# Kernel tuning notes

Measured on AMD Instinct MI355X. Metric: run time of the kernel, lower is better.

The kernel has to match this reference:

```python
import jax, jax.numpy as jnp
import numpy as np

EPS = 1e-7
MAX_TANH = 1.0 - 1e-6  # clamp for arctanh stability


def _norm(v):
    # last-axis L2 norm, clamped away from zero
    return jnp.maximum(jnp.linalg.norm(v, axis=-1, keepdims=True), EPS)


def log_map_zero(y):
    # Poincare ball (c=1) log map at the origin
    n = _norm(y)
    return jnp.arctanh(jnp.clip(n, 0.0, MAX_TANH)) * y / n


def exp_map_zero(v):
    # Poincare ball (c=1) exp map at the origin
    n = _norm(v)
    return jnp.tanh(n) * v / n


def h_add(x, y):
    # Mobius addition x (+) y on the Poincare ball (c=1)
    xy = jnp.sum(x * y, axis=-1, keepdims=True)
    x2 = jnp.sum(x * x, axis=-1, keepdims=True)
    y2 = jnp.sum(y * y, axis=-1, keepdims=True)
    num = (1.0 + 2.0 * xy + y2) * x + (1.0 - x2) * y
    den = 1.0 + 2.0 * xy + x2 * y2
    return num / jnp.maximum(den, EPS)


def h_mul(x, W):
    # Mobius matrix-vector multiply: exp0( log0(x) @ W )
    return exp_map_zero(log_map_zero(x) @ W)


def setup_inputs() -> dict:
    key = jax.random.key(0)
    k1, k2, k3, k4 = jax.random.split(key, 4)
    N, F_IN, F_OUT = 8192, 128, 128
    # node features inside the unit ball: ||x|| ~ 0.05*sqrt(128) ~ 0.57
    x = 0.05 * jax.random.normal(k1, (N, F_IN), dtype=jnp.float32)
    # sparse-ish row-normalized dense adjacency
    a = (jax.random.uniform(k2, (N, N)) < 0.01).astype(jnp.float32)
    adj = a / jnp.maximum(a.sum(axis=1, keepdims=True), 1.0)
    # xavier-uniform-ish weights
    lim_e = np.sqrt(6.0 / (F_IN + F_IN)) * np.sqrt(2.0)
    lim_l = np.sqrt(6.0 / (2 * F_IN + F_OUT)) * np.sqrt(2.0)
    embed = jax.random.uniform(k3, (F_IN, F_IN), minval=-lim_e, maxval=lim_e, dtype=jnp.float32)
    layer = jax.random.uniform(k4, (2 * F_IN, F_OUT), minval=-lim_l, maxval=lim_l, dtype=jnp.float32)
    embed_bias = jnp.zeros((F_IN,), dtype=jnp.float32)
    layer_bias = jnp.zeros((F_OUT,), dtype=jnp.float32)
    return {"x": x, "adj": adj, "embed": embed, "layer": layer,
            "embed_bias": embed_bias, "layer_bias": layer_bias}


def reference(x, adj, embed, layer, embed_bias, layer_bias):
    # h = (embed (x)mobius x) (+) embed_bias
    h = h_mul(x, embed)                      # [N, F_IN]
    h = h_add(h, embed_bias[None, :])
    # neighbor aggregation in tangent space at origin
    neigh = exp_map_zero(adj @ log_map_zero(h))   # [N, F_IN]
    # out = (layer (x)mobius [x ; neigh]) (+) layer_bias
    out = h_mul(jnp.concatenate((x, neigh), axis=1), layer)  # [N, F_OUT]
    out = h_add(out, layer_bias[None, :])
    return out
```

## Files before the change

### kernel.cpp

```cpp
#include <hip/hip_runtime.h>
#include <math.h>

#define EPS  1e-7f
#define MAXT 0.999999f

typedef short  s16x8  __attribute__((ext_vector_type(8)));
typedef float  f32x16 __attribute__((ext_vector_type(16)));

__device__ __forceinline__ float waveRedSum(float v) {
    #pragma unroll
    for (int off = 32; off > 0; off >>= 1)
        v += __shfl_xor(v, off, 64);
    return v;
}

__device__ __forceinline__ unsigned short f2bf(float f) {
    unsigned u = __float_as_uint(f);
    u += 0x7fff + ((u >> 16) & 1);
    return (unsigned short)(u >> 16);
}

__global__ __launch_bounds__(256) void kA(const float* __restrict__ x,
                                          const float* __restrict__ embed,
                                          const float* __restrict__ ebias,
                                          unsigned short* __restrict__ vpack) {
    __shared__ float u[4][128];
    const int wave = threadIdx.x >> 6;
    const int lane = threadIdx.x & 63;
    const int row  = blockIdx.x * 4 + wave;
    const int c0   = lane * 2;

    const float2 xr = *(const float2*)(x + (size_t)row * 128 + c0);

    float n2 = waveRedSum(xr.x * xr.x + xr.y * xr.y);
    float n  = fmaxf(sqrtf(n2), EPS);
    float sc = atanhf(fminf(n, MAXT)) / n;
    u[wave][c0]     = xr.x * sc;
    u[wave][c0 + 1] = xr.y * sc;
    __syncthreads();

    float a0 = 0.f, a1 = 0.f;
    #pragma unroll 8
    for (int k = 0; k < 128; k++) {
        float  uk = u[wave][k];
        float2 e  = *(const float2*)(embed + (size_t)k * 128 + c0);
        a0 = fmaf(uk, e.x, a0);
        a1 = fmaf(uk, e.y, a1);
    }

    float np2 = waveRedSum(a0 * a0 + a1 * a1);
    float np  = fmaxf(sqrtf(np2), EPS);
    float se  = tanhf(np) / np;
    float h0 = a0 * se, h1 = a1 * se;
    float x2 = np2 * se * se;

    float bx = ebias[c0], by = ebias[c0 + 1];
    float xy = waveRedSum(h0 * bx + h1 * by);
    float y2 = waveRedSum(bx * bx + by * by);
    float den = fmaxf(1.f + 2.f * xy + x2 * y2, EPS);
    float cx = 1.f + 2.f * xy + y2;
    float cy = 1.f - x2;
    float hb0 = (cx * h0 + cy * bx) / den;
    float hb1 = (cx * h1 + cy * by) / den;

    float m2 = waveRedSum(hb0 * hb0 + hb1 * hb1);
    float m  = fmaxf(sqrtf(m2), EPS);
    float sl = atanhf(fminf(m, MAXT)) / m;
    float v0 = hb0 * sl, v1 = hb1 * sl;

    const int tbase = (row >> 4) * 2048 + (row & 15);
    vpack[tbase + c0 * 16]       = f2bf(v0);
    vpack[tbase + (c0 + 1) * 16] = f2bf(v1);
}

__device__ __forceinline__ void kb_chunk(const float4& ca0, const float4& ca1,
                                         const unsigned short* bp,
                                         f32x16& acc0, f32x16& acc1,
                                         f32x16& acc2, f32x16& acc3) {
    s16x8 b0 = *(const s16x8*)(bp);
    s16x8 b1 = *(const s16x8*)(bp + 32 * 16);
    s16x8 b2 = *(const s16x8*)(bp + 64 * 16);
    s16x8 b3 = *(const s16x8*)(bp + 96 * 16);
    union { unsigned short u[8]; s16x8 v; } af;
    af.u[0] = f2bf(ca0.x); af.u[1] = f2bf(ca0.y);
    af.u[2] = f2bf(ca0.z); af.u[3] = f2bf(ca0.w);
    af.u[4] = f2bf(ca1.x); af.u[5] = f2bf(ca1.y);
    af.u[6] = f2bf(ca1.z); af.u[7] = f2bf(ca1.w);
    acc0 = __builtin_amdgcn_mfma_f32_32x32x16_bf16(af.v, b0, acc0, 0, 0, 0);
    acc1 = __builtin_amdgcn_mfma_f32_32x32x16_bf16(af.v, b1, acc1, 0, 0, 0);
    acc2 = __builtin_amdgcn_mfma_f32_32x32x16_bf16(af.v, b2, acc2, 0, 0, 0);
    acc3 = __builtin_amdgcn_mfma_f32_32x32x16_bf16(af.v, b3, acc3, 0, 0, 0);
}

__global__ __launch_bounds__(256) void kB(const float* __restrict__ adj,
                                          const unsigned short* __restrict__ vpack,
                                          float* __restrict__ tpart,
                                          int klen) {
    const int wave = threadIdx.x >> 6;
    const int lane = threadIdx.x & 63;
    const int rt   = blockIdx.x * 4 + wave;
    const int r0   = rt * 32;
    const int k0   = blockIdx.y * klen;
    float* tout    = tpart + (size_t)blockIdx.y * (8192 * 128);

    const int m  = lane & 31;
    const int kh = lane >> 5;

    const float* aptr = adj + (size_t)(r0 + m) * 8192 + k0 + kh * 8;
    const unsigned short* bbase = vpack + (size_t)(k0 >> 4) * 2048 + m * 16 + kh * 8;

    f32x16 acc0 = {0.f}, acc1 = {0.f}, acc2 = {0.f}, acc3 = {0.f};

    const int kiters = klen >> 4;

    float4 a0 = *(const float4*)(aptr);
    float4 a1 = *(const float4*)(aptr + 4);

    for (int kt = 0; kt < kiters - 1; ++kt) {
        float4 ca0 = a0, ca1 = a1;
        aptr += 16;
        a0 = *(const float4*)(aptr);
        a1 = *(const float4*)(aptr + 4);
        kb_chunk(ca0, ca1, bbase + (size_t)kt * 2048, acc0, acc1, acc2, acc3);
    }
    kb_chunk(a0, a1, bbase + (size_t)(kiters - 1) * 2048, acc0, acc1, acc2, acc3);

    #pragma unroll
    for (int r = 0; r < 16; ++r) {
        int row  = r0 + (r & 3) + 8 * (r >> 2) + 4 * kh;
        float* o = tout + (size_t)row * 128 + m;
        o[0]  = acc0[r];
        o[32] = acc1[r];
        o[64] = acc2[r];
        o[96] = acc3[r];
    }
}

__global__ __launch_bounds__(256) void kC(const float* __restrict__ x,
                                          const float* __restrict__ tpart,
                                          const float* __restrict__ layer,
                                          const float* __restrict__ lbias,
                                          float* __restrict__ out,
                                          int S) {
    __shared__ float w[4][256];
    const int wave = threadIdx.x >> 6;
    const int lane = threadIdx.x & 63;
    const int row  = blockIdx.x * 4 + wave;
    const int c0   = lane * 2;

    float2 tr = *(const float2*)(tpart + (size_t)row * 128 + c0);
    for (int s = 1; s < S; s++) {
        float2 p = *(const float2*)(tpart + (size_t)s * 8192 * 128 + (size_t)row * 128 + c0);
        tr.x += p.x; tr.y += p.y;
    }
    const float2 xr = *(const float2*)(x + (size_t)row * 128 + c0);

    float st = waveRedSum(tr.x * tr.x + tr.y * tr.y);
    float sx = waveRedSum(xr.x * xr.x + xr.y * xr.y);

    float nt = fmaxf(sqrtf(st), EPS);
    float se = tanhf(nt) / nt;

    float ncat2 = sx + st * se * se;
    float ncat  = fmaxf(sqrtf(ncat2), EPS);
    float sw    = atanhf(fminf(ncat, MAXT)) / ncat;
    w[wave][c0]           = xr.x * sw;
    w[wave][c0 + 1]       = xr.y * sw;
    w[wave][128 + c0]     = tr.x * se * sw;
    w[wave][128 + c0 + 1] = tr.y * se * sw;
    __syncthreads();

    float a0 = 0.f, a1 = 0.f;
    #pragma unroll 8
    for (int k = 0; k < 256; k++) {
        float  wk = w[wave][k];
        float2 e  = *(const float2*)(layer + (size_t)k * 128 + c0);
        a0 = fmaf(wk, e.x, a0);
        a1 = fmaf(wk, e.y, a1);
    }

    float np2 = waveRedSum(a0 * a0 + a1 * a1);
    float np  = fmaxf(sqrtf(np2), EPS);
    float so  = tanhf(np) / np;
    float o0 = a0 * so, o1 = a1 * so;
    float x2 = np2 * so * so;

    float bx = lbias[c0], by = lbias[c0 + 1];
    float xy = waveRedSum(o0 * bx + o1 * by);
    float y2 = waveRedSum(bx * bx + by * by);
    float den = fmaxf(1.f + 2.f * xy + x2 * y2, EPS);
    float cx = 1.f + 2.f * xy + y2;
    float cy = 1.f - x2;

    float2 res;
    res.x = (cx * o0 + cy * bx) / den;
    res.y = (cx * o1 + cy * by) / den;
    *(float2*)(out + (size_t)row * 128 + c0) = res;
}

extern "C" void kernel_launch(void* const* d_in, const int* in_sizes, int n_in,
                              void* d_out, int out_size, void* d_ws, size_t ws_size,
                              hipStream_t stream) {
    const float* x     = (const float*)d_in[0];
    const float* adj   = (const float*)d_in[1];
    const float* embed = (const float*)d_in[2];
    const float* layer = (const float*)d_in[3];
    const float* eb    = (const float*)d_in[4];
    const float* lb    = (const float*)d_in[5];
    float* out = (float*)d_out;

    const size_t vbytes = (size_t)8192 * 128 * 2;
    const size_t slice  = (size_t)8192 * 128 * 4;

    int S = 1;
    if      (ws_size >= vbytes + 16 * slice) S = 16;
    else if (ws_size >= vbytes +  8 * slice) S = 8;
    else if (ws_size >= vbytes +  4 * slice) S = 4;
    else if (ws_size >= vbytes +  2 * slice) S = 2;

    unsigned short* vpack = (unsigned short*)d_ws;
    float* tpart = (float*)((char*)d_ws + vbytes);

    kA<<<2048, 256, 0, stream>>>(x, embed, eb, vpack);
    kB<<<dim3(64, S), 256, 0, stream>>>(adj, vpack, tpart, 8192 / S);
    kC<<<2048, 256, 0, stream>>>(x, tpart, layer, lb, out, S);
}
```

Before: 519.5 us.

## Deepen kB software pipeline with multi-stage A/B prefetch and cap split-K at 8

Rewrites the kB inner loop to keep four adjacency chunks and two B chunks in flight in registers, unrolled by four, so global-load latency is hidden behind the MFMAs. The fp32-to-bf16 conversion now uses the packed __float22bfloat162_rn intrinsic in place of manual per-element rounding. The split-K factor is capped at 8, which halves the partial-sum traffic in kC but gives kB fewer blocks. The change raises register pressure, and at the tail it issues redundant clamped loads.

New measurement: 530.3 us. 1.02x slower.

```diff
diff --git a/kernel.cpp b/kernel.cpp
--- a/kernel.cpp
+++ b/kernel.cpp
@@ -1,4 +1,5 @@
 #include <hip/hip_runtime.h>
+#include <hip/hip_bf16.h>
 #include <math.h>
 
 #define EPS  1e-7f
@@ -6,6 +7,7 @@
 
 typedef short  s16x8  __attribute__((ext_vector_type(8)));
 typedef float  f32x16 __attribute__((ext_vector_type(16)));
+typedef float  f32x4  __attribute__((ext_vector_type(4)));
 
 __device__ __forceinline__ float waveRedSum(float v) {
     #pragma unroll
@@ -73,23 +75,13 @@
     vpack[tbase + (c0 + 1) * 16] = f2bf(v1);
 }
 
-__device__ __forceinline__ void kb_chunk(const float4& ca0, const float4& ca1,
-                                         const unsigned short* bp,
-                                         f32x16& acc0, f32x16& acc1,
-                                         f32x16& acc2, f32x16& acc3) {
-    s16x8 b0 = *(const s16x8*)(bp);
-    s16x8 b1 = *(const s16x8*)(bp + 32 * 16);
-    s16x8 b2 = *(const s16x8*)(bp + 64 * 16);
-    s16x8 b3 = *(const s16x8*)(bp + 96 * 16);
-    union { unsigned short u[8]; s16x8 v; } af;
-    af.u[0] = f2bf(ca0.x); af.u[1] = f2bf(ca0.y);
-    af.u[2] = f2bf(ca0.z); af.u[3] = f2bf(ca0.w);
-    af.u[4] = f2bf(ca1.x); af.u[5] = f2bf(ca1.y);
-    af.u[6] = f2bf(ca1.z); af.u[7] = f2bf(ca1.w);
-    acc0 = __builtin_amdgcn_mfma_f32_32x32x16_bf16(af.v, b0, acc0, 0, 0, 0);
-    acc1 = __builtin_amdgcn_mfma_f32_32x32x16_bf16(af.v, b1, acc1, 0, 0, 0);
-    acc2 = __builtin_amdgcn_mfma_f32_32x32x16_bf16(af.v, b2, acc2, 0, 0, 0);
-    acc3 = __builtin_amdgcn_mfma_f32_32x32x16_bf16(af.v, b3, acc3, 0, 0, 0);
+__device__ __forceinline__ s16x8 pack_bf16x8(const f32x4 a, const f32x4 b) {
+    union { __hip_bfloat162 h[4]; s16x8 v; } r;
+    r.h[0] = __float22bfloat162_rn({a.x, a.y});
+    r.h[1] = __float22bfloat162_rn({a.z, a.w});
+    r.h[2] = __float22bfloat162_rn({b.x, b.y});
+    r.h[3] = __float22bfloat162_rn({b.z, b.w});
+    return r.v;
 }
 
 __global__ __launch_bounds__(256) void kB(const float* __restrict__ adj,
@@ -106,24 +98,55 @@
     const int m  = lane & 31;
     const int kh = lane >> 5;
 
-    const float* aptr = adj + (size_t)(r0 + m) * 8192 + k0 + kh * 8;
+    const float* abase = adj + (size_t)(r0 + m) * 8192 + k0 + kh * 8;
     const unsigned short* bbase = vpack + (size_t)(k0 >> 4) * 2048 + m * 16 + kh * 8;
 
+    const int kiters = klen >> 4;
+
     f32x16 acc0 = {0.f}, acc1 = {0.f}, acc2 = {0.f}, acc3 = {0.f};
 
-    const int kiters = klen >> 4;
-
-    float4 a0 = *(const float4*)(aptr);
-    float4 a1 = *(const float4*)(aptr + 4);
-
-    for (int kt = 0; kt < kiters - 1; ++kt) {
-        float4 ca0 = a0, ca1 = a1;
-        aptr += 16;
-        a0 = *(const float4*)(aptr);
-        a1 = *(const float4*)(aptr + 4);
-        kb_chunk(ca0, ca1, bbase + (size_t)kt * 2048, acc0, acc1, acc2, acc3);
-    }
-    kb_chunk(a0, a1, bbase + (size_t)(kiters - 1) * 2048, acc0, acc1, acc2, acc3);
+    f32x4 aq[4][2];
+    s16x8 bq[2][4];
+
+    #pragma unroll
+    for (int c = 0; c < 4; ++c) {
+        aq[c][0] = *(const f32x4*)(abase + c * 16);
+        aq[c][1] = *(const f32x4*)(abase + c * 16 + 4);
+    }
+    #pragma unroll
+    for (int c = 0; c < 2; ++c) {
+        const unsigned short* bp = bbase + (size_t)c * 2048;
+        bq[c][0] = *(const s16x8*)(bp);
+        bq[c][1] = *(const s16x8*)(bp + 512);
+        bq[c][2] = *(const s16x8*)(bp + 1024);
+        bq[c][3] = *(const s16x8*)(bp + 1536);
+    }
+
+    for (int it = 0; it < kiters; it += 4) {
+        #pragma unroll
+        for (int u = 0; u < 4; ++u) {
+            const int c = it + u;
+            s16x8 af = pack_bf16x8(aq[u][0], aq[u][1]);
+            acc0 = __builtin_amdgcn_mfma_f32_32x32x16_bf16(af, bq[u & 1][0], acc0, 0, 0, 0);
+            acc1 = __builtin_amdgcn_mfma_f32_32x32x16_bf16(af, bq[u & 1][1], acc1, 0, 0, 0);
+            acc2 = __builtin_amdgcn_mfma_f32_32x32x16_bf16(af, bq[u & 1][2], acc2, 0, 0, 0);
+            acc3 = __builtin_amdgcn_mfma_f32_32x32x16_bf16(af, bq[u & 1][3], acc3, 0, 0, 0);
+
+            {
+                const int cb = min(c + 2, kiters - 1);
+                const unsigned short* bp = bbase + (size_t)cb * 2048;
+                bq[u & 1][0] = *(const s16x8*)(bp);
+                bq[u & 1][1] = *(const s16x8*)(bp + 512);
+                bq[u & 1][2] = *(const s16x8*)(bp + 1024);
+                bq[u & 1][3] = *(const s16x8*)(bp + 1536);
+            }
+            {
+                const int ca = min(c + 4, kiters - 1);
+                aq[u][0] = *(const f32x4*)(abase + (size_t)ca * 16);
+                aq[u][1] = *(const f32x4*)(abase + (size_t)ca * 16 + 4);
+            }
+        }
+    }
 
     #pragma unroll
     for (int r = 0; r < 16; ++r) {
@@ -213,10 +236,9 @@
     const size_t slice  = (size_t)8192 * 128 * 4;
 
     int S = 1;
-    if      (ws_size >= vbytes + 16 * slice) S = 16;
-    else if (ws_size >= vbytes +  8 * slice) S = 8;
-    else if (ws_size >= vbytes +  4 * slice) S = 4;
-    else if (ws_size >= vbytes +  2 * slice) S = 2;
+    if      (ws_size >= vbytes + 8 * slice) S = 8;
+    else if (ws_size >= vbytes + 4 * slice) S = 4;
+    else if (ws_size >= vbytes + 2 * slice) S = 2;
 
     unsigned short* vpack = (unsigned short*)d_ws;
     float* tpart = (float*)((char*)d_ws + vbytes);
```
